# Kernel optimization log

Hardware: AMD Instinct MI355X
Metric: run time of the kernel (lower is better)

The kernel has to match this reference:

```python
import jax, jax.numpy as jnp
import numpy as np


def setup_inputs() -> dict:
    key = jax.random.key(0)
    k1, k2, k3 = jax.random.split(key, 3)
    shape = (1, 48, 64, 128, 1)  # [B, D/4, H/4, W/4, C=1] cost volume
    return {
        "c1": jax.random.normal(k1, shape, dtype=jnp.float32),
        "c2": jax.random.normal(k2, shape, dtype=jnp.float32),
        "c3": jax.random.normal(k3, shape, dtype=jnp.float32),
    }


def _regress(c):
    # UpSampling3D(4): nearest-neighbor repeat along D, H, W -> [B, D, H, W, 1]
    x = jnp.repeat(jnp.repeat(jnp.repeat(c, 4, axis=1), 4, axis=2), 4, axis=3)
    # all-ones 4x4x4 box filter, stride 1, SAME padding (TF pads lo=1, hi=2;
    # lax 'SAME' matches this split for even kernels)
    filt = jnp.ones((4, 4, 4, 1, 1), dtype=x.dtype)  # DHWIO
    x = jax.lax.conv_general_dilated(
        x, filt, window_strides=(1, 1, 1), padding="SAME",
        dimension_numbers=("NDHWC", "DHWIO", "NDHWC"))
    x = jnp.squeeze(x, -1)  # [B, D, H, W]
    # soft-argmin over disparity axis
    w = jax.nn.softmax(x, axis=1)
    disp = jnp.arange(x.shape[1], dtype=x.dtype)[None, :, None, None]
    return jnp.sum(w * disp, axis=1)  # [B, H, W]


def reference(c1, c2, c3):
    # inference path (training=None): only c3 is processed
    return _regress(c3)
```

## Files before the change

### kernel.cpp

```cpp
#include <hip/hip_runtime.h>


#define DC 48
#define HC 64
#define WC 128
#define WOUT 512
#define NOUT (256 * 512)

__device__ __forceinline__ void axis_weights(int p, int& off, float& w0, float& w1) {
    off = (p == 0) ? -1 : 0;
    w0  = (p == 0) ? 1.f : (p == 1) ? 4.f : (p == 2) ? 3.f : 2.f;
    w1  = (p == 0) ? 3.f : (p == 1) ? 0.f : (p == 2) ? 1.f : 2.f;
}

__global__ __launch_bounds__(256)
void regress_kernel(const float* __restrict__ c3, float* __restrict__ out) {
    int t = blockIdx.x * blockDim.x + threadIdx.x;
    int w = t & (WOUT - 1);
    int h = t >> 9;

    int jh = h >> 2, ph = h & 3;
    int jw = w >> 2, pw = w & 3;

    int offh, offw;
    float whA, whB, wwA, wwB;
    axis_weights(ph, offh, whA, whB);
    axis_weights(pw, offw, wwA, wwB);

    int jh0 = jh + offh, jh1 = jh0 + 1;
    float wh0 = (jh0 >= 0 && jh0 < HC) ? whA : 0.f;
    float wh1 = (jh1 < HC) ? whB : 0.f;
    jh0 = (jh0 < 0) ? 0 : jh0;
    jh1 = (jh1 > HC - 1) ? HC - 1 : jh1;

    int jw0 = jw + offw, jw1 = jw0 + 1;
    float ww0 = (jw0 >= 0 && jw0 < WC) ? wwA : 0.f;
    float ww1 = (jw1 < WC) ? wwB : 0.f;
    jw0 = (jw0 < 0) ? 0 : jw0;
    jw1 = (jw1 > WC - 1) ? WC - 1 : jw1;

    float w00 = wh0 * ww0, w01 = wh0 * ww1, w10 = wh1 * ww0, w11 = wh1 * ww1;

    int i00 = jh0 * WC + jw0, i01 = jh0 * WC + jw1;
    int i10 = jh1 * WC + jw0, i11 = jh1 * WC + jw1;

    float S[DC];
    #pragma unroll
    for (int jd = 0; jd < DC; ++jd) {
        const float* p = c3 + jd * (HC * WC);
        S[jd] = w00 * p[i00] + w01 * p[i01] + w10 * p[i10] + w11 * p[i11];
    }

    float m = -1e30f;
    #pragma unroll
    for (int jd = 0; jd < DC; ++jd) {
        float Sm = (jd == 0) ? 0.f : S[jd - 1];
        float Sc = S[jd];
        float Sp = (jd == DC - 1) ? 0.f : S[jd + 1];
        float x0 = Sm + 3.f * Sc;
        float x1 = 4.f * Sc;
        float x2 = 3.f * Sc + Sp;
        float x3 = 2.f * Sc + 2.f * Sp;
        m = fmaxf(m, fmaxf(fmaxf(x0, x1), fmaxf(x2, x3)));
    }

    float s = 0.f, sd = 0.f;
    #pragma unroll
    for (int jd = 0; jd < DC; ++jd) {
        float Sm = (jd == 0) ? 0.f : S[jd - 1];
        float Sc = S[jd];
        float Sp = (jd == DC - 1) ? 0.f : S[jd + 1];
        float x0 = Sm + 3.f * Sc;
        float x1 = 4.f * Sc;
        float x2 = 3.f * Sc + Sp;
        float x3 = 2.f * Sc + 2.f * Sp;
        float e0 = __expf(x0 - m);
        float e1 = __expf(x1 - m);
        float e2 = __expf(x2 - m);
        float e3 = __expf(x3 - m);
        s += e0 + e1 + e2 + e3;
        float d0 = (float)(4 * jd);
        sd = fmaf(e0, d0, sd);
        sd = fmaf(e1, d0 + 1.f, sd);
        sd = fmaf(e2, d0 + 2.f, sd);
        sd = fmaf(e3, d0 + 3.f, sd);
    }

    out[t] = sd / s;
}

extern "C" void kernel_launch(void* const* d_in, const int* in_sizes, int n_in,
                              void* d_out, int out_size, void* d_ws, size_t ws_size,
                              hipStream_t stream) {
    (void)in_sizes; (void)n_in; (void)d_ws; (void)ws_size; (void)out_size;
    const float* c3 = (const float*)d_in[2];
    float* out = (float*)d_out;
    regress_kernel<<<NOUT / 256, 256, 0, stream>>>(c3, out);
}
```

Baseline: 65.95 us.

## Split disparity axis across four lanes per pixel with shuffle reductions

Each output pixel is now handled by four lanes of a wavefront, each covering 12 of the 48 coarse disparity slices plus halo slices. The max, sum and weighted sum are combined with cross-lane xor shuffles. This cuts per-thread register use (S shrinks from 48 to 14 floats) and raises the thread count fourfold for more parallelism. It also folds log2(e) into the filter weights so exp2 can be used directly. The cost is redundant halo loads, extra shuffles, and only a quarter of lanes writing output.

```diff
diff --git a/kernel.cpp b/kernel.cpp
--- a/kernel.cpp
+++ b/kernel.cpp
@@ -5,7 +5,9 @@
 #define HC 64
 #define WC 128
 #define WOUT 512
-#define NOUT (256 * 512)
+#define HOUT 256
+#define NPIX (HOUT * WOUT)
+#define LOG2E 1.4426950408889634f
 
 __device__ __forceinline__ void axis_weights(int p, int& off, float& w0, float& w1) {
     off = (p == 0) ? -1 : 0;
@@ -15,9 +17,14 @@
 
 __global__ __launch_bounds__(256)
 void regress_kernel(const float* __restrict__ c3, float* __restrict__ out) {
-    int t = blockIdx.x * blockDim.x + threadIdx.x;
-    int w = t & (WOUT - 1);
-    int h = t >> 9;
+    int lane = threadIdx.x & 63;
+    int px   = lane & 15;
+    int q    = lane >> 4;
+    int wv   = threadIdx.x >> 6;
+    int g    = blockIdx.x * 64 + wv * 16 + px;
+
+    int w = g & (WOUT - 1);
+    int h = g >> 9;
 
     int jh = h >> 2, ph = h & 3;
     int jw = w >> 2, pw = w & 3;
@@ -39,54 +46,62 @@
     jw0 = (jw0 < 0) ? 0 : jw0;
     jw1 = (jw1 > WC - 1) ? WC - 1 : jw1;
 
-    float w00 = wh0 * ww0, w01 = wh0 * ww1, w10 = wh1 * ww0, w11 = wh1 * ww1;
+    float w00 = wh0 * ww0 * LOG2E, w01 = wh0 * ww1 * LOG2E;
+    float w10 = wh1 * ww0 * LOG2E, w11 = wh1 * ww1 * LOG2E;
 
     int i00 = jh0 * WC + jw0, i01 = jh0 * WC + jw1;
     int i10 = jh1 * WC + jw0, i11 = jh1 * WC + jw1;
 
-    float S[DC];
+    int base = 12 * q;
+    float S[14];
     #pragma unroll
-    for (int jd = 0; jd < DC; ++jd) {
-        const float* p = c3 + jd * (HC * WC);
-        S[jd] = w00 * p[i00] + w01 * p[i01] + w10 * p[i10] + w11 * p[i11];
+    for (int kk = 0; kk < 14; ++kk) {
+        int jd  = base - 1 + kk;
+        bool ok = (jd >= 0) && (jd < DC);
+        int jc  = ok ? jd : 0;
+        const float* p = c3 + jc * (HC * WC);
+        float val = w00 * p[i00] + w01 * p[i01] + w10 * p[i10] + w11 * p[i11];
+        S[kk] = ok ? val : 0.f;
     }
 
     float m = -1e30f;
     #pragma unroll
-    for (int jd = 0; jd < DC; ++jd) {
-        float Sm = (jd == 0) ? 0.f : S[jd - 1];
-        float Sc = S[jd];
-        float Sp = (jd == DC - 1) ? 0.f : S[jd + 1];
+    for (int i = 0; i < 12; ++i) {
+        float Sm = S[i], Sc = S[i + 1], Sp = S[i + 2];
         float x0 = Sm + 3.f * Sc;
         float x1 = 4.f * Sc;
         float x2 = 3.f * Sc + Sp;
         float x3 = 2.f * Sc + 2.f * Sp;
         m = fmaxf(m, fmaxf(fmaxf(x0, x1), fmaxf(x2, x3)));
     }
+    m = fmaxf(m, __shfl_xor(m, 16, 64));
+    m = fmaxf(m, __shfl_xor(m, 32, 64));
 
     float s = 0.f, sd = 0.f;
     #pragma unroll
-    for (int jd = 0; jd < DC; ++jd) {
-        float Sm = (jd == 0) ? 0.f : S[jd - 1];
-        float Sc = S[jd];
-        float Sp = (jd == DC - 1) ? 0.f : S[jd + 1];
+    for (int i = 0; i < 12; ++i) {
+        float Sm = S[i], Sc = S[i + 1], Sp = S[i + 2];
         float x0 = Sm + 3.f * Sc;
         float x1 = 4.f * Sc;
         float x2 = 3.f * Sc + Sp;
         float x3 = 2.f * Sc + 2.f * Sp;
-        float e0 = __expf(x0 - m);
-        float e1 = __expf(x1 - m);
-        float e2 = __expf(x2 - m);
-        float e3 = __expf(x3 - m);
+        float e0 = __builtin_amdgcn_exp2f(x0 - m);
+        float e1 = __builtin_amdgcn_exp2f(x1 - m);
+        float e2 = __builtin_amdgcn_exp2f(x2 - m);
+        float e3 = __builtin_amdgcn_exp2f(x3 - m);
         s += e0 + e1 + e2 + e3;
-        float d0 = (float)(4 * jd);
+        float d0 = (float)(4 * (base + i));
         sd = fmaf(e0, d0, sd);
         sd = fmaf(e1, d0 + 1.f, sd);
         sd = fmaf(e2, d0 + 2.f, sd);
         sd = fmaf(e3, d0 + 3.f, sd);
     }
+    s  += __shfl_xor(s, 16, 64);
+    s  += __shfl_xor(s, 32, 64);
+    sd += __shfl_xor(sd, 16, 64);
+    sd += __shfl_xor(sd, 32, 64);
 
-    out[t] = sd / s;
+    if (q == 0) out[g] = sd / s;
 }
 
 extern "C" void kernel_launch(void* const* d_in, const int* in_sizes, int n_in,
@@ -95,5 +110,5 @@
     (void)in_sizes; (void)n_in; (void)d_ws; (void)ws_size; (void)out_size;
     const float* c3 = (const float*)d_in[2];
     float* out = (float*)d_out;
-    regress_kernel<<<NOUT / 256, 256, 0, stream>>>(c3, out);
+    regress_kernel<<<NPIX / 64, 256, 0, stream>>>(c3, out);
 }
```

New measurement: 66.99 us. About the same (+1.6%).

## Tile output 16x16 per block with shared-memory separable box filter

Applied to the files above, without the earlier changes.

Each block now handles a 16x16 output tile. It stages the 6x6xD coarse-cost halo in shared memory, applies the W-axis weights once into a second shared buffer, then each thread applies the H-axis weights. This replaces the 4 scattered global loads per depth level per thread with reuse from LDS. The LOG2E scale is also folded into the weights so the code can call the hardware exp2 directly. The cost is two barriers plus LDS traffic, and the 2D block index remaps the output writes.

```diff
diff --git a/kernel.cpp b/kernel.cpp
--- a/kernel.cpp
+++ b/kernel.cpp
@@ -5,51 +5,60 @@
 #define HC 64
 #define WC 128
 #define WOUT 512
-#define NOUT (256 * 512)
-
-__device__ __forceinline__ void axis_weights(int p, int& off, float& w0, float& w1) {
-    off = (p == 0) ? -1 : 0;
-    w0  = (p == 0) ? 1.f : (p == 1) ? 4.f : (p == 2) ? 3.f : 2.f;
-    w1  = (p == 0) ? 3.f : (p == 1) ? 0.f : (p == 2) ? 1.f : 2.f;
-}
+#define HOUT 256
+#define LOG2E 1.4426950408889634f
 
 __global__ __launch_bounds__(256)
 void regress_kernel(const float* __restrict__ c3, float* __restrict__ out) {
-    int t = blockIdx.x * blockDim.x + threadIdx.x;
-    int w = t & (WOUT - 1);
-    int h = t >> 9;
+    __shared__ float Ct[DC][6][6];
+    __shared__ float Bt[DC][6][16];
 
-    int jh = h >> 2, ph = h & 3;
-    int jw = w >> 2, pw = w & 3;
+    int tid = threadIdx.x;
+    int bx = blockIdx.x & 31;
+    int by = blockIdx.x >> 5;
+    int W0 = bx * 16, H0 = by * 16;
+    int JW0 = bx * 4 - 1, JH0 = by * 4 - 1;
 
-    int offh, offw;
-    float whA, whB, wwA, wwB;
-    axis_weights(ph, offh, whA, whB);
-    axis_weights(pw, offw, wwA, wwB);
+    #pragma unroll
+    for (int k = 0; k < 7; ++k) {
+        int idx = tid + k * 256;
+        if (idx < DC * 36) {
+            int jd  = idx / 36;
+            int rem = idx - jd * 36;
+            int r   = rem / 6;
+            int c   = rem - r * 6;
+            int gh = JH0 + r, gw = JW0 + c;
+            bool ok = (gh >= 0) && (gh < HC) && (gw >= 0) && (gw < WC);
+            ((float*)Ct)[idx] = ok ? c3[jd * (HC * WC) + gh * WC + gw] : 0.f;
+        }
+    }
+    __syncthreads();
 
-    int jh0 = jh + offh, jh1 = jh0 + 1;
-    float wh0 = (jh0 >= 0 && jh0 < HC) ? whA : 0.f;
-    float wh1 = (jh1 < HC) ? whB : 0.f;
-    jh0 = (jh0 < 0) ? 0 : jh0;
-    jh1 = (jh1 > HC - 1) ? HC - 1 : jh1;
+    #pragma unroll
+    for (int k = 0; k < 18; ++k) {
+        int idx = tid + k * 256;
+        int jd  = idx / 96;
+        int rem = idx - jd * 96;
+        int r   = rem >> 4;
+        int x   = rem & 15;
+        int pw  = x & 3;
+        int jwA = (x >> 2) + 1 + ((pw == 0) ? -1 : 0);
+        float wwA = ((pw == 0) ? 1.f : (pw == 1) ? 4.f : (pw == 2) ? 3.f : 2.f) * LOG2E;
+        float wwB = ((pw == 0) ? 3.f : (pw == 1) ? 0.f : (pw == 2) ? 1.f : 2.f) * LOG2E;
+        ((float*)Bt)[idx] = wwA * Ct[jd][r][jwA] + wwB * Ct[jd][r][jwA + 1];
+    }
+    __syncthreads();
 
-    int jw0 = jw + offw, jw1 = jw0 + 1;
-    float ww0 = (jw0 >= 0 && jw0 < WC) ? wwA : 0.f;
-    float ww1 = (jw1 < WC) ? wwB : 0.f;
-    jw0 = (jw0 < 0) ? 0 : jw0;
-    jw1 = (jw1 > WC - 1) ? WC - 1 : jw1;
-
-    float w00 = wh0 * ww0, w01 = wh0 * ww1, w10 = wh1 * ww0, w11 = wh1 * ww1;
-
-    int i00 = jh0 * WC + jw0, i01 = jh0 * WC + jw1;
-    int i10 = jh1 * WC + jw0, i11 = jh1 * WC + jw1;
+    int tx = tid & 15, ty = tid >> 4;
+    int ph = ty & 3;
+    int rA = (ty >> 2) + 1 + ((ph == 0) ? -1 : 0);
+    float whA = (ph == 0) ? 1.f : (ph == 1) ? 4.f : (ph == 2) ? 3.f : 2.f;
+    float whB = (ph == 0) ? 3.f : (ph == 1) ? 0.f : (ph == 2) ? 1.f : 2.f;
 
     float S[DC];
     #pragma unroll
-    for (int jd = 0; jd < DC; ++jd) {
-        const float* p = c3 + jd * (HC * WC);
-        S[jd] = w00 * p[i00] + w01 * p[i01] + w10 * p[i10] + w11 * p[i11];
-    }
+    for (int jd = 0; jd < DC; ++jd)
+        S[jd] = whA * Bt[jd][rA][tx] + whB * Bt[jd][rA + 1][tx];
 
     float m = -1e30f;
     #pragma unroll
@@ -74,10 +83,10 @@
         float x1 = 4.f * Sc;
         float x2 = 3.f * Sc + Sp;
         float x3 = 2.f * Sc + 2.f * Sp;
-        float e0 = __expf(x0 - m);
-        float e1 = __expf(x1 - m);
-        float e2 = __expf(x2 - m);
-        float e3 = __expf(x3 - m);
+        float e0 = __builtin_amdgcn_exp2f(x0 - m);
+        float e1 = __builtin_amdgcn_exp2f(x1 - m);
+        float e2 = __builtin_amdgcn_exp2f(x2 - m);
+        float e3 = __builtin_amdgcn_exp2f(x3 - m);
         s += e0 + e1 + e2 + e3;
         float d0 = (float)(4 * jd);
         sd = fmaf(e0, d0, sd);
@@ -86,7 +95,7 @@
         sd = fmaf(e3, d0 + 3.f, sd);
     }
 
-    out[t] = sd / s;
+    out[(H0 + ty) * WOUT + W0 + tx] = sd / s;
 }
 
 extern "C" void kernel_launch(void* const* d_in, const int* in_sizes, int n_in,
@@ -95,5 +104,5 @@
     (void)in_sizes; (void)n_in; (void)d_ws; (void)ws_size; (void)out_size;
     const float* c3 = (const float*)d_in[2];
     float* out = (float*)d_out;
-    regress_kernel<<<NOUT / 256, 256, 0, stream>>>(c3, out);
+    regress_kernel<<<(HOUT / 16) * (WOUT / 16), 256, 0, stream>>>(c3, out);
 }
```

Result: slower. 67.63 us (+2.6%).
